# Optimization experiments

Measured on AMD Instinct MI355X. Metric: run time of the kernel, lower is better.

Reference implementation:

```python
import jax, jax.numpy as jnp
import numpy as np

K = 0.1
GAMMA = 1.0


def setup_inputs() -> dict:
    key = jax.random.key(0)
    k1, k2, k3, k4, k5 = jax.random.split(key, 5)
    N, M, D = 16384, 2048, 128
    # Points must lie inside the Poincare ball (0 < norm < 1) for acos/asin validity.
    x = jax.random.normal(k1, (N, D), dtype=jnp.float32)
    x = x / jnp.linalg.norm(x, axis=1, keepdims=True)
    x = x * jax.random.uniform(k2, (N, 1), minval=0.3, maxval=0.9, dtype=jnp.float32)
    p = jax.random.normal(k3, (M, D), dtype=jnp.float32)
    p = p / jnp.linalg.norm(p, axis=1, keepdims=True)
    p = p * jax.random.uniform(k4, (M, 1), minval=0.3, maxval=0.9, dtype=jnp.float32)
    labels = jax.random.randint(k5, (N,), 0, M)
    return {"x": x, "p": p, "labels": labels}


def reference(x, p, labels):
    N = x.shape[0]
    dot = x @ p.T                                   # [N, M], replaces NxMxD broadcast
    nx2 = jnp.sum(x * x, axis=1, keepdims=True)     # [N, 1] = ||x||^2
    np2 = jnp.sum(p * p, axis=1)                    # [M]    = ||p||^2
    np_norm = jnp.sqrt(np2)                         # [M]

    num = dot * (1.0 + np2) - np2 * (1.0 + nx2)     # [N, M]
    # Faithful to original: sum of squared pairwise distances over the BATCH axis (dim=0)
    # sum_i ||x_i - p_j||^2 = sum_i||x_i||^2 + N*||p_j||^2 - 2*(sum_i x_i)@p_j
    sum_sq_dist = jnp.sum(nx2) + N * np2 - 2.0 * (jnp.sum(x, axis=0) @ p.T)  # [M]
    den = np_norm * jnp.sqrt(sum_sq_dist) * jnp.sqrt(1.0 + np2 * nx2 - 2.0 * dot)  # [N, M]
    angle = jnp.arccos(num / den)                   # [N, M]

    psi = jnp.arcsin(K * (1.0 - np2) / np_norm)     # [M], broadcast over rows
    angles = jnp.maximum(0.0, angle - psi)          # [N, M]

    rows = jnp.arange(N)
    positive = angles[rows, labels]                 # [N]
    neg = jnp.maximum(0.0, GAMMA - angles)          # [N, M]
    negative = jnp.sum(neg, axis=1) - neg[rows, labels]  # exclude label column
    return jnp.mean(positive + negative)
```

## Files before the change

### kernel.cpp

```cpp
#include <hip/hip_runtime.h>
#include <math.h>

#define KCONST 0.1f
#define GAMMA_C 1.0f
#define D_DIM 128

typedef __attribute__((ext_vector_type(4))) float f32x4;

#define ASYNC_COPY16(gsrc, ldst)                                                  \
  __builtin_amdgcn_global_load_lds(                                               \
      (const __attribute__((address_space(1))) void*)(gsrc),                      \
      (__attribute__((address_space(3))) void*)(ldst), 16, 0, 0)

#define FP8_SCALE 16.0f
#define INV_TWO_OVER_SQ 0.0078125f

__device__ __forceinline__ int pk_fp8x4(float a, float b, float c, float d) {
  int v = __builtin_amdgcn_cvt_pk_fp8_f32(a, b, 0, 0);
  v = __builtin_amdgcn_cvt_pk_fp8_f32(c, d, v, 1);
  return v;
}

__global__ void prep_x(const float* __restrict__ x, unsigned char* __restrict__ xb,
                       float* __restrict__ nx2p, float* __restrict__ pSumX,
                       float* __restrict__ pS2, float* __restrict__ out_zero, int N) {
  if (blockIdx.x == 0 && threadIdx.x == 0) *out_zero = 0.f;
  const int tid = threadIdx.x;
  const int l = tid & 63, w = tid >> 6;
  const int l16 = l & 15, sub = l >> 4;
  const int waveId = blockIdx.x * 4 + w;
  const float4* x4 = (const float4*)x;
  float4 c0 = {0.f, 0.f, 0.f, 0.f}, c1 = {0.f, 0.f, 0.f, 0.f};
  float s2 = 0.f;
#pragma unroll
  for (int it = 0; it < 4; ++it) {
    int row = (waveId + it * 1024) * 4 + sub;
    float4 v0 = x4[row * 32 + 2 * l16];
    float4 v1 = x4[row * 32 + 2 * l16 + 1];
    c0.x += v0.x; c0.y += v0.y; c0.z += v0.z; c0.w += v0.w;
    c1.x += v1.x; c1.y += v1.y; c1.z += v1.z; c1.w += v1.w;
    int2 st;
    st.x = pk_fp8x4(v0.x * FP8_SCALE, v0.y * FP8_SCALE, v0.z * FP8_SCALE, v0.w * FP8_SCALE);
    st.y = pk_fp8x4(v1.x * FP8_SCALE, v1.y * FP8_SCALE, v1.z * FP8_SCALE, v1.w * FP8_SCALE);
    *(int2*)(xb + (size_t)row * 128 + 8 * l16) = st;
    float sq = v0.x * v0.x;
    sq = fmaf(v0.y, v0.y, sq); sq = fmaf(v0.z, v0.z, sq); sq = fmaf(v0.w, v0.w, sq);
    sq = fmaf(v1.x, v1.x, sq); sq = fmaf(v1.y, v1.y, sq);
    sq = fmaf(v1.z, v1.z, sq); sq = fmaf(v1.w, v1.w, sq);
    sq += __shfl_down(sq, 8); sq += __shfl_down(sq, 4);
    sq += __shfl_down(sq, 2); sq += __shfl_down(sq, 1);
    if (l16 == 0) {
      nx2p[row] = 1.f + sq;
      s2 += sq;
    }
  }
  s2 += __shfl_down(s2, 16);
  s2 += __shfl_down(s2, 32);
  __shared__ float cs[128];
  __shared__ float s2w[4];
  if (tid < 128) cs[tid] = 0.f;
  if (l == 0) s2w[w] = s2;
  __syncthreads();
  atomicAdd(&cs[8 * l16 + 0], c0.x); atomicAdd(&cs[8 * l16 + 1], c0.y);
  atomicAdd(&cs[8 * l16 + 2], c0.z); atomicAdd(&cs[8 * l16 + 3], c0.w);
  atomicAdd(&cs[8 * l16 + 4], c1.x); atomicAdd(&cs[8 * l16 + 5], c1.y);
  atomicAdd(&cs[8 * l16 + 6], c1.z); atomicAdd(&cs[8 * l16 + 7], c1.w);
  __syncthreads();
  if (tid < 128) pSumX[blockIdx.x * 128 + tid] = cs[tid];
  if (tid == 0) pS2[blockIdx.x] = s2w[0] + s2w[1] + s2w[2] + s2w[3];
}

__global__ void merge_sums(const float* __restrict__ pSumX, const float* __restrict__ pS2,
                           float* __restrict__ sum_x, float* __restrict__ sum_nx2) {
  __shared__ float seg[8][128];
  __shared__ float s2w[4];
  const int t = threadIdx.x;
  const int col = t & 127;
  const int sg = t >> 7;
  float s = 0.f;
#pragma unroll
  for (int b = 0; b < 32; ++b) s += pSumX[(sg * 32 + b) * 128 + col];
  seg[sg][col] = s;
  float s2 = (t < 256) ? pS2[t] : 0.f;
  if (t < 256) {
#pragma unroll
    for (int off = 32; off; off >>= 1) s2 += __shfl_down(s2, off);
    if ((t & 63) == 0) s2w[t >> 6] = s2;
  }
  __syncthreads();
  if (t < 128) {
    float r = 0.f;
#pragma unroll
    for (int k = 0; k < 8; ++k) r += seg[k][col];
    sum_x[t] = r;
  }
  if (t == 0) sum_nx2[0] = s2w[0] + s2w[1] + s2w[2] + s2w[3];
}

__global__ void prep_p(const float* __restrict__ p, unsigned char* __restrict__ pb,
                       const float* __restrict__ sum_x, const float* __restrict__ sum_nx2,
                       float4* __restrict__ colc, float* __restrict__ psiA,
                       int M, int N) {
  const int tid = threadIdx.x;
  const int l = tid & 63, w = tid >> 6;
  const int l16 = l & 15, sub = l >> 4;
  const int j = blockIdx.x * 16 + w * 4 + sub;
  const float4* p4 = (const float4*)p;
  float4 v0 = p4[j * 32 + 2 * l16];
  float4 v1 = p4[j * 32 + 2 * l16 + 1];
  int2 st;
  st.x = pk_fp8x4(v0.x * FP8_SCALE, v0.y * FP8_SCALE, v0.z * FP8_SCALE, v0.w * FP8_SCALE);
  st.y = pk_fp8x4(v1.x * FP8_SCALE, v1.y * FP8_SCALE, v1.z * FP8_SCALE, v1.w * FP8_SCALE);
  *(int2*)(pb + (size_t)j * 128 + 8 * l16) = st;
  float np2 = v0.x * v0.x;
  np2 = fmaf(v0.y, v0.y, np2); np2 = fmaf(v0.z, v0.z, np2); np2 = fmaf(v0.w, v0.w, np2);
  np2 = fmaf(v1.x, v1.x, np2); np2 = fmaf(v1.y, v1.y, np2);
  np2 = fmaf(v1.z, v1.z, np2); np2 = fmaf(v1.w, v1.w, np2);
  const float4 sx0 = *(const float4*)&sum_x[8 * l16];
  const float4 sx1 = *(const float4*)&sum_x[8 * l16 + 4];
  float sd = v0.x * sx0.x;
  sd = fmaf(v0.y, sx0.y, sd); sd = fmaf(v0.z, sx0.z, sd); sd = fmaf(v0.w, sx0.w, sd);
  sd = fmaf(v1.x, sx1.x, sd); sd = fmaf(v1.y, sx1.y, sd);
  sd = fmaf(v1.z, sx1.z, sd); sd = fmaf(v1.w, sx1.w, sd);
#pragma unroll
  for (int off = 8; off; off >>= 1) {
    np2 += __shfl_down(np2, off);
    sd += __shfl_down(sd, off);
  }
  if (l16 == 0) {
    float ssd = *sum_nx2 + (float)N * np2 - 2.f * sd;
    float npn = sqrtf(np2);
    float cfi = 1.f / (npn * sqrtf(ssd));
    float4 cc;
    cc.x = (1.f + np2) * cfi * (1.0f / 256.0f);
    cc.y = np2 * cfi;
    cc.z = np2;
    cc.w = 256.0f * np2 / (1.f + np2);
    colc[j] = cc;
    psiA[j] = asinf(KCONST * (1.f - np2) / npn);
  }
}

__global__ __launch_bounds__(256, 4) void pair_mfma(
    const unsigned char* __restrict__ xb, const unsigned char* __restrict__ pb,
    const int* __restrict__ labels, const float* __restrict__ nx2p,
    const float4* __restrict__ colc, const float* __restrict__ psiA,
    float* __restrict__ out, float invN) {
  __shared__ float4 xs4[1024];
  __shared__ float4 ps4[2][512];
  __shared__ float wred[4];

  const int b = blockIdx.x;
  const int rowTile = b >> 2;
  const int cg = b & 3;
  const int row0 = rowTile * 128;

  const int tid = threadIdx.x;
  const int l = tid & 63;
  const int w = tid >> 6;
  const float4* xg = (const float4*)(xb + (size_t)row0 * 128);

#pragma unroll
  for (int ci = w; ci < 16; ci += 4) {
    int qi = ci * 64 + l;
    int r = qi >> 3, ql = qi & 7;
    ASYNC_COPY16(xg + r * 8 + (ql ^ (r & 7)), xs4 + ci * 64);
  }
  {
    const float4* pg = (const float4*)(pb + (size_t)(cg * 8) * 64 * 128);
#pragma unroll
    for (int ci = w; ci < 8; ci += 4) {
      int qi = ci * 64 + l;
      int r = qi >> 3, ql = qi & 7;
      ASYNC_COPY16(pg + r * 8 + (ql ^ (r & 7)), ps4[0] + ci * 64);
    }
  }

  const int m = tid & 15;
  const int q = (tid >> 4) & 3;
  const int wr = (w & 1) * 64;
  const int wc = (w >> 1) * 32;

  f32x4 rnp4v[4];
  int4 lb4v[4];
#pragma unroll
  for (int r = 0; r < 4; ++r) {
    rnp4v[r] = __builtin_bit_cast(f32x4, *(const float4*)&nx2p[row0 + wr + r * 16 + q * 4]);
    lb4v[r] = *(const int4*)&labels[row0 + wr + r * 16 + q * 4];
  }

  float4 ccur0 = colc[(cg * 8) * 64 + wc + m];
  float4 ccur1 = colc[(cg * 8) * 64 + wc + 16 + m];

  const char* xsb = (const char*)xs4;
  float ssum = 0.f;
#pragma unroll
  for (int it = 0; it < 8; ++it) {
    __syncthreads();
    const int cur = it & 1;
    if (it < 7) {
      const float4* pg = (const float4*)(pb + (size_t)(cg * 8 + it + 1) * 64 * 128);
#pragma unroll
      for (int ci = w; ci < 8; ci += 4) {
        int qi = ci * 64 + l;
        int r = qi >> 3, ql = qi & 7;
        ASYNC_COPY16(pg + r * 8 + (ql ^ (r & 7)), ps4[cur ^ 1] + ci * 64);
      }
    }
    float4 cnext0, cnext1;
    if (it < 7) {
      cnext0 = colc[(cg * 8 + it + 1) * 64 + wc + m];
      cnext1 = colc[(cg * 8 + it + 1) * 64 + wc + 16 + m];
    }

    const char* psb = (const char*)ps4[cur];
    f32x4 acc[4][2];
#pragma unroll
    for (int r = 0; r < 4; ++r) {
      acc[r][0] = (f32x4)(0.f);
      acc[r][1] = (f32x4)(0.f);
    }
#pragma unroll
    for (int s = 0; s < 4; ++s) {
      const int g = s * 4 + q;
      const int gq = g >> 1, gh = (g & 1) << 3;
      long a[4], bf[2];
#pragma unroll
      for (int c = 0; c < 2; ++c) {
        const int row = wc + c * 16 + m;
        bf[c] = *(const long*)(psb + row * 128 + ((gq ^ (row & 7)) << 4) + gh);
      }
#pragma unroll
      for (int r = 0; r < 4; ++r) {
        const int row = wr + r * 16 + m;
        a[r] = *(const long*)(xsb + row * 128 + ((gq ^ (row & 7)) << 4) + gh);
      }
#pragma unroll
      for (int r = 0; r < 4; ++r)
#pragma unroll
        for (int c = 0; c < 2; ++c)
          acc[r][c] = __builtin_amdgcn_mfma_f32_16x16x32_fp8_fp8(a[r], bf[c], acc[r][c], 0, 0, 0);
    }

    const int ct0 = (cg * 8 + it) * 64;
#pragma unroll
    for (int c = 0; c < 2; ++c) {
      const int col = ct0 + wc + c * 16 + m;
      const float4 cc = (c == 0) ? ccur0 : ccur1;
      const float Tc = cc.w;
#pragma unroll
      for (int r = 0; r < 4; ++r) {
        const f32x4 rnp4 = rnp4v[r];
        const int4 lb4 = lb4v[r];
        const f32x4 dv = acc[r][c];
        float e0 = fmaf(-Tc, rnp4[0], dv[0]);
        float e1 = fmaf(-Tc, rnp4[1], dv[1]);
        float e2 = fmaf(-Tc, rnp4[2], dv[2]);
        float e3 = fmaf(-Tc, rnp4[3], dv[3]);
        float hm = fmaxf(fmaxf(e0, e1), fmaxf(e2, e3));
        bool h = (hm > 0.f) | (col == lb4.x) | (col == lb4.y) |
                 (col == lb4.z) | (col == lb4.w);
        if (__builtin_expect(h, 0)) {
          const float psi = psiA[col];
          const float C1 = 1.f + psi;
          const float omnp2 = 1.f - cc.z;
#pragma unroll
          for (int g2 = 0; g2 < 4; ++g2) {
            float rnp = rnp4[g2];
            float dotRaw = dv[g2];
            int lb = (g2 == 0) ? lb4.x : (g2 == 1) ? lb4.y : (g2 == 2) ? lb4.z : lb4.w;
            float den2 = fmaf(-INV_TWO_OVER_SQ, dotRaw, fmaf(cc.z, rnp, omnp2));
            float nump = fmaf(dotRaw, cc.x, -cc.y * rnp);
            float u = nump * __builtin_amdgcn_rsqf(den2);
            u = __builtin_amdgcn_fmed3f(u, -1.f, 1.f);
            float ax = fabsf(u);
            float rt = __builtin_amdgcn_sqrtf(1.f - ax);
            float poly = fmaf(fmaf(fmaf(-0.0187293f, ax, 0.0742610f), ax, -0.2121144f),
                              ax, 1.5707288f);
            float ac = rt * poly;
            ac = (u >= 0.f) ? ac : 3.14159265358979f - ac;
            float neg = __builtin_amdgcn_fmed3f(C1 - ac, 0.f, 1.f);
            float pos = fmaxf(0.f, ac - psi);
            ssum += (col == lb) ? pos : neg;
          }
        }
      }
    }
    if (it < 7) {
      ccur0 = cnext0;
      ccur1 = cnext1;
    }
  }

#pragma unroll
  for (int off = 32; off; off >>= 1) ssum += __shfl_down(ssum, off);
  if (l == 0) wred[w] = ssum;
  __syncthreads();
  if (tid == 0)
    atomicAdd(out, (wred[0] + wred[1] + wred[2] + wred[3]) * invN);
}

extern "C" void kernel_launch(void* const* d_in, const int* in_sizes, int n_in,
                              void* d_out, int out_size, void* d_ws, size_t ws_size,
                              hipStream_t stream) {
  const float* x = (const float*)d_in[0];
  const float* p = (const float*)d_in[1];
  const int* labels = (const int*)d_in[2];
  float* out = (float*)d_out;
  const int N = in_sizes[2];
  const int M = in_sizes[1] / D_DIM;

  float* ws = (float*)d_ws;
  float* nx2p = ws;
  float4* colc = (float4*)(ws + N);
  float* psiA = ws + N + 4 * M;
  unsigned char* xb = (unsigned char*)(ws + N + 5 * M);
  unsigned char* pb = (unsigned char*)(ws + N + 5 * M + 32 * N);
  float* pSumX = ws + N + 5 * M + 32 * N + 32 * M;
  float* pS2 = pSumX + 256 * 128;
  float* sum_x = pS2 + 256;
  float* sum_nx2 = sum_x + 128;

  prep_x<<<256, 256, 0, stream>>>(x, xb, nx2p, pSumX, pS2, out, N);
  merge_sums<<<1, 1024, 0, stream>>>(pSumX, pS2, sum_x, sum_nx2);
  prep_p<<<M / 16, 256, 0, stream>>>(p, pb, sum_x, sum_nx2, colc, psiA, M, N);

  pair_mfma<<<512, 256, 0, stream>>>(xb, pb, labels, nx2p, colc, psiA, out,
                                     1.0f / (float)N);
}
```

Before: 93.28 us.

## Fold merge_sums into prep_p and stage P tiles per-wave via registers

Removes the single-block merge_sums launch: prep_x now runs 512 blocks, and every prep_p block re-reduces the 512 partial sums itself. In pair_mfma, the block-wide async LDS copy of each P tile with a __syncthreads per iteration becomes per-wave register prefetch into private double-buffered LDS slices. Each wave only touches its own slice, so the per-iteration block barrier goes away. The costs are a redundant partial-sum reduction in all 128 prep_p blocks, more register pressure, and launch bounds lowered from 4 to 3 waves per SIMD.

```diff
diff --git a/kernel.cpp b/kernel.cpp
--- a/kernel.cpp
+++ b/kernel.cpp
@@ -33,8 +33,8 @@
   float4 c0 = {0.f, 0.f, 0.f, 0.f}, c1 = {0.f, 0.f, 0.f, 0.f};
   float s2 = 0.f;
 #pragma unroll
-  for (int it = 0; it < 4; ++it) {
-    int row = (waveId + it * 1024) * 4 + sub;
+  for (int it = 0; it < 2; ++it) {
+    int row = (waveId + it * 2048) * 4 + sub;
     float4 v0 = x4[row * 32 + 2 * l16];
     float4 v1 = x4[row * 32 + 2 * l16 + 1];
     c0.x += v0.x; c0.y += v0.y; c0.z += v0.z; c0.w += v0.w;
@@ -70,38 +70,30 @@
   if (tid == 0) pS2[blockIdx.x] = s2w[0] + s2w[1] + s2w[2] + s2w[3];
 }
 
-__global__ void merge_sums(const float* __restrict__ pSumX, const float* __restrict__ pS2,
-                           float* __restrict__ sum_x, float* __restrict__ sum_nx2) {
-  __shared__ float seg[8][128];
-  __shared__ float s2w[4];
-  const int t = threadIdx.x;
-  const int col = t & 127;
-  const int sg = t >> 7;
-  float s = 0.f;
-#pragma unroll
-  for (int b = 0; b < 32; ++b) s += pSumX[(sg * 32 + b) * 128 + col];
-  seg[sg][col] = s;
-  float s2 = (t < 256) ? pS2[t] : 0.f;
-  if (t < 256) {
-#pragma unroll
-    for (int off = 32; off; off >>= 1) s2 += __shfl_down(s2, off);
-    if ((t & 63) == 0) s2w[t >> 6] = s2;
-  }
-  __syncthreads();
-  if (t < 128) {
-    float r = 0.f;
-#pragma unroll
-    for (int k = 0; k < 8; ++k) r += seg[k][col];
-    sum_x[t] = r;
-  }
-  if (t == 0) sum_nx2[0] = s2w[0] + s2w[1] + s2w[2] + s2w[3];
-}
-
 __global__ void prep_p(const float* __restrict__ p, unsigned char* __restrict__ pb,
-                       const float* __restrict__ sum_x, const float* __restrict__ sum_nx2,
+                       const float* __restrict__ pSumX, const float* __restrict__ pS2,
                        float4* __restrict__ colc, float* __restrict__ psiA,
                        int M, int N) {
+  __shared__ float seg[2][128];
+  __shared__ float sumx_s[128];
+  __shared__ float s2_s;
   const int tid = threadIdx.x;
+  {
+    const int c = tid & 127, sg = tid >> 7;
+    float s = 0.f;
+#pragma unroll 16
+    for (int bb = sg * 256; bb < sg * 256 + 256; ++bb) s += pSumX[bb * 128 + c];
+    seg[sg][c] = s;
+    float s2 = pS2[tid] + pS2[tid + 256];
+#pragma unroll
+    for (int off = 32; off; off >>= 1) s2 += __shfl_down(s2, off);
+    __shared__ float s2w[4];
+    if ((tid & 63) == 0) s2w[tid >> 6] = s2;
+    __syncthreads();
+    if (tid < 128) sumx_s[tid] = seg[0][tid] + seg[1][tid];
+    if (tid == 0) s2_s = s2w[0] + s2w[1] + s2w[2] + s2w[3];
+    __syncthreads();
+  }
   const int l = tid & 63, w = tid >> 6;
   const int l16 = l & 15, sub = l >> 4;
   const int j = blockIdx.x * 16 + w * 4 + sub;
@@ -116,8 +108,8 @@
   np2 = fmaf(v0.y, v0.y, np2); np2 = fmaf(v0.z, v0.z, np2); np2 = fmaf(v0.w, v0.w, np2);
   np2 = fmaf(v1.x, v1.x, np2); np2 = fmaf(v1.y, v1.y, np2);
   np2 = fmaf(v1.z, v1.z, np2); np2 = fmaf(v1.w, v1.w, np2);
-  const float4 sx0 = *(const float4*)&sum_x[8 * l16];
-  const float4 sx1 = *(const float4*)&sum_x[8 * l16 + 4];
+  const float4 sx0 = *(const float4*)&sumx_s[8 * l16];
+  const float4 sx1 = *(const float4*)&sumx_s[8 * l16 + 4];
   float sd = v0.x * sx0.x;
   sd = fmaf(v0.y, sx0.y, sd); sd = fmaf(v0.z, sx0.z, sd); sd = fmaf(v0.w, sx0.w, sd);
   sd = fmaf(v1.x, sx1.x, sd); sd = fmaf(v1.y, sx1.y, sd);
@@ -128,7 +120,7 @@
     sd += __shfl_down(sd, off);
   }
   if (l16 == 0) {
-    float ssd = *sum_nx2 + (float)N * np2 - 2.f * sd;
+    float ssd = s2_s + (float)N * np2 - 2.f * sd;
     float npn = sqrtf(np2);
     float cfi = 1.f / (npn * sqrtf(ssd));
     float4 cc;
@@ -141,13 +133,13 @@
   }
 }
 
-__global__ __launch_bounds__(256, 4) void pair_mfma(
+__global__ __launch_bounds__(256, 3) void pair_mfma(
     const unsigned char* __restrict__ xb, const unsigned char* __restrict__ pb,
     const int* __restrict__ labels, const float* __restrict__ nx2p,
     const float4* __restrict__ colc, const float* __restrict__ psiA,
     float* __restrict__ out, float invN) {
   __shared__ float4 xs4[1024];
-  __shared__ float4 ps4[2][512];
+  __shared__ float4 psw[4][2][256];
   __shared__ float wred[4];
 
   const int b = blockIdx.x;
@@ -166,20 +158,23 @@
     int r = qi >> 3, ql = qi & 7;
     ASYNC_COPY16(xg + r * 8 + (ql ^ (r & 7)), xs4 + ci * 64);
   }
-  {
-    const float4* pg = (const float4*)(pb + (size_t)(cg * 8) * 64 * 128);
-#pragma unroll
-    for (int ci = w; ci < 8; ci += 4) {
-      int qi = ci * 64 + l;
-      int r = qi >> 3, ql = qi & 7;
-      ASYNC_COPY16(pg + r * 8 + (ql ^ (r & 7)), ps4[0] + ci * 64);
-    }
-  }
 
   const int m = tid & 15;
   const int q = (tid >> 4) & 3;
   const int wr = (w & 1) * 64;
   const int wc = (w >> 1) * 32;
+  const int lrow = l >> 1;
+  const int h = l & 1;
+  char* buf0 = (char*)psw[w][0];
+  char* buf1 = (char*)psw[w][1];
+
+  float4 v0[4];
+  {
+    const float4* pg =
+        (const float4*)(pb + (size_t)((cg * 8) * 64 + wc + lrow) * 128 + h * 64);
+#pragma unroll
+    for (int k = 0; k < 4; ++k) v0[k] = pg[k];
+  }
 
   f32x4 rnp4v[4];
   int4 lb4v[4];
@@ -188,32 +183,34 @@
     rnp4v[r] = __builtin_bit_cast(f32x4, *(const float4*)&nx2p[row0 + wr + r * 16 + q * 4]);
     lb4v[r] = *(const int4*)&labels[row0 + wr + r * 16 + q * 4];
   }
-
   float4 ccur0 = colc[(cg * 8) * 64 + wc + m];
   float4 ccur1 = colc[(cg * 8) * 64 + wc + 16 + m];
 
+#pragma unroll
+  for (int k = 0; k < 4; ++k) {
+    int qq = h * 4 + k;
+    *(float4*)(buf0 + lrow * 128 + ((qq ^ (lrow & 7)) << 4)) = v0[k];
+  }
+  __syncthreads();
+
   const char* xsb = (const char*)xs4;
   float ssum = 0.f;
 #pragma unroll
-  for (int it = 0; it < 8; ++it) {
-    __syncthreads();
-    const int cur = it & 1;
-    if (it < 7) {
-      const float4* pg = (const float4*)(pb + (size_t)(cg * 8 + it + 1) * 64 * 128);
-#pragma unroll
-      for (int ci = w; ci < 8; ci += 4) {
-        int qi = ci * 64 + l;
-        int r = qi >> 3, ql = qi & 7;
-        ASYNC_COPY16(pg + r * 8 + (ql ^ (r & 7)), ps4[cur ^ 1] + ci * 64);
-      }
-    }
+  for (int t = 0; t < 8; ++t) {
+    const char* cur = (t & 1) ? buf1 : buf0;
+    char* nxt = (t & 1) ? buf0 : buf1;
+
+    float4 vn[4];
     float4 cnext0, cnext1;
-    if (it < 7) {
-      cnext0 = colc[(cg * 8 + it + 1) * 64 + wc + m];
-      cnext1 = colc[(cg * 8 + it + 1) * 64 + wc + 16 + m];
-    }
-
-    const char* psb = (const char*)ps4[cur];
+    if (t < 7) {
+      const float4* pg = (const float4*)(
+          pb + (size_t)((cg * 8 + t + 1) * 64 + wc + lrow) * 128 + h * 64);
+#pragma unroll
+      for (int k = 0; k < 4; ++k) vn[k] = pg[k];
+      cnext0 = colc[(cg * 8 + t + 1) * 64 + wc + m];
+      cnext1 = colc[(cg * 8 + t + 1) * 64 + wc + 16 + m];
+    }
+
     f32x4 acc[4][2];
 #pragma unroll
     for (int r = 0; r < 4; ++r) {
@@ -227,8 +224,8 @@
       long a[4], bf[2];
 #pragma unroll
       for (int c = 0; c < 2; ++c) {
-        const int row = wc + c * 16 + m;
-        bf[c] = *(const long*)(psb + row * 128 + ((gq ^ (row & 7)) << 4) + gh);
+        const int lr = c * 16 + m;
+        bf[c] = *(const long*)(cur + lr * 128 + ((gq ^ (lr & 7)) << 4) + gh);
       }
 #pragma unroll
       for (int r = 0; r < 4; ++r) {
@@ -242,7 +239,7 @@
           acc[r][c] = __builtin_amdgcn_mfma_f32_16x16x32_fp8_fp8(a[r], bf[c], acc[r][c], 0, 0, 0);
     }
 
-    const int ct0 = (cg * 8 + it) * 64;
+    const int ct0 = (cg * 8 + t) * 64;
 #pragma unroll
     for (int c = 0; c < 2; ++c) {
       const int col = ct0 + wc + c * 16 + m;
@@ -258,9 +255,9 @@
         float e2 = fmaf(-Tc, rnp4[2], dv[2]);
         float e3 = fmaf(-Tc, rnp4[3], dv[3]);
         float hm = fmaxf(fmaxf(e0, e1), fmaxf(e2, e3));
-        bool h = (hm > 0.f) | (col == lb4.x) | (col == lb4.y) |
-                 (col == lb4.z) | (col == lb4.w);
-        if (__builtin_expect(h, 0)) {
+        bool hh = (hm > 0.f) | (col == lb4.x) | (col == lb4.y) |
+                  (col == lb4.z) | (col == lb4.w);
+        if (__builtin_expect(hh, 0)) {
           const float psi = psiA[col];
           const float C1 = 1.f + psi;
           const float omnp2 = 1.f - cc.z;
@@ -286,7 +283,13 @@
         }
       }
     }
-    if (it < 7) {
+
+    if (t < 7) {
+#pragma unroll
+      for (int k = 0; k < 4; ++k) {
+        int qq = h * 4 + k;
+        *(float4*)(nxt + lrow * 128 + ((qq ^ (lrow & 7)) << 4)) = vn[k];
+      }
       ccur0 = cnext0;
       ccur1 = cnext1;
     }
@@ -317,13 +320,10 @@
   unsigned char* xb = (unsigned char*)(ws + N + 5 * M);
   unsigned char* pb = (unsigned char*)(ws + N + 5 * M + 32 * N);
   float* pSumX = ws + N + 5 * M + 32 * N + 32 * M;
-  float* pS2 = pSumX + 256 * 128;
-  float* sum_x = pS2 + 256;
-  float* sum_nx2 = sum_x + 128;
-
-  prep_x<<<256, 256, 0, stream>>>(x, xb, nx2p, pSumX, pS2, out, N);
-  merge_sums<<<1, 1024, 0, stream>>>(pSumX, pS2, sum_x, sum_nx2);
-  prep_p<<<M / 16, 256, 0, stream>>>(p, pb, sum_x, sum_nx2, colc, psiA, M, N);
+  float* pS2 = pSumX + 512 * 128;
+
+  prep_x<<<512, 256, 0, stream>>>(x, xb, nx2p, pSumX, pS2, out, N);
+  prep_p<<<M / 16, 256, 0, stream>>>(p, pb, pSumX, pS2, colc, psiA, M, N);
 
   pair_mfma<<<512, 256, 0, stream>>>(xb, pb, labels, nx2p, colc, psiA, out,
                                      1.0f / (float)N);
```

Result: no change. 93.35 us (+0.1%).
